# Kernel tuning notes

Hardware: AMD Instinct MI355X
Metric: run time of the kernel (lower is better)

Reference implementation:

```python
import jax, jax.numpy as jnp
import numpy as np

B, T = 4, 2048
N_EMBD = 1024
TIME_EMBD = 128
N_HEAD = 16
C_IN = N_EMBD + TIME_EMBD  # 1152


def setup_inputs() -> dict:
    key = jax.random.key(0)
    ks = jax.random.split(key, 7)
    s_in = 1.0 / np.sqrt(C_IN)
    s_e = 1.0 / np.sqrt(N_EMBD)
    return {
        "x": jax.random.normal(ks[0], (B, T, C_IN), jnp.float32),
        "ln_w": jnp.ones((C_IN,), jnp.float32),
        "ln_b": jnp.zeros((C_IN,), jnp.float32),
        "W_attn": jax.random.normal(ks[1], (C_IN, 3 * N_EMBD), jnp.float32) * s_in,
        "b_attn": jax.random.normal(ks[2], (3 * N_EMBD,), jnp.float32) * 0.01,
        "W_proj": jax.random.normal(ks[3], (N_EMBD, N_EMBD), jnp.float32) * s_e,
        "b_proj": jax.random.normal(ks[4], (N_EMBD,), jnp.float32) * 0.01,
    }


def _layernorm(x, w, b, eps=1e-5):
    mu = jnp.mean(x, axis=-1, keepdims=True)
    var = jnp.var(x, axis=-1, keepdims=True)
    return (x - mu) * jax.lax.rsqrt(var + eps) * w + b


def reference(x, ln_w, ln_b, W_attn, b_attn, W_proj, b_proj):
    h = _layernorm(x, ln_w, ln_b)                      # [B,T,C_IN]
    qkv = h @ W_attn + b_attn                          # [B,T,3*N_EMBD]
    q, k, v = jnp.split(qkv, 3, axis=-1)
    hd = N_EMBD // N_HEAD
    q = q.reshape(B, T, N_HEAD, hd).transpose(0, 2, 1, 3)  # [B,H,T,hd]
    k = k.reshape(B, T, N_HEAD, hd).transpose(0, 2, 1, 3)
    v = v.reshape(B, T, N_HEAD, hd).transpose(0, 2, 1, 3)
    att = jnp.einsum("bhqd,bhkd->bhqk", q, k) * (1.0 / np.sqrt(hd))
    mask = jnp.tril(jnp.ones((T, T), bool))
    att = jnp.where(mask, att, -jnp.inf)
    att = jax.nn.softmax(att, axis=-1)                 # dropout p=0 -> identity
    y = jnp.einsum("bhqk,bhkd->bhqd", att, v)          # [B,H,T,hd]
    y = y.transpose(0, 2, 1, 3).reshape(B, T, N_EMBD)
    return y @ W_proj + b_proj
```

## Files before the change

kernel.cpp:

```cpp
#include <hip/hip_runtime.h>
#include <hip/hip_bf16.h>

#define BB 4
#define TT 2048
#define C_IN 1152
#define NE 1024
#define NH 16
#define HD 64
#define MM (BB*TT)
#define N_QKV (3*NE)

typedef __attribute__((ext_vector_type(8))) short s16x8;
typedef __attribute__((ext_vector_type(4))) float f32x4;

static __device__ __forceinline__ unsigned short f2bf(float x) {
    unsigned int u = __float_as_uint(x);
    unsigned int r = (u + 0x7fffu + ((u >> 16) & 1u)) >> 16;
    return (unsigned short)r;
}

static __device__ __forceinline__ void async16(const void* g, void* l) {
    __builtin_amdgcn_global_load_lds((const __attribute__((address_space(1))) void*)g,
                                     (__attribute__((address_space(3))) void*)l, 16, 0, 0);
}

__global__ __launch_bounds__(256) void ln_kernel(const float* __restrict__ x,
                                                 const float* __restrict__ w,
                                                 const float* __restrict__ b,
                                                 unsigned short* __restrict__ h) {
    const int row = blockIdx.x;
    const float* xr = x + (size_t)row * C_IN;
    float s = 0.f, sq = 0.f;
    for (int i = threadIdx.x; i < C_IN; i += 256) {
        float v = xr[i];
        s += v; sq += v * v;
    }
    for (int off = 1; off < 64; off <<= 1) {
        s  += __shfl_xor(s, off, 64);
        sq += __shfl_xor(sq, off, 64);
    }
    __shared__ float red[2][4];
    const int wid = threadIdx.x >> 6, lane = threadIdx.x & 63;
    if (lane == 0) { red[0][wid] = s; red[1][wid] = sq; }
    __syncthreads();
    s  = red[0][0] + red[0][1] + red[0][2] + red[0][3];
    sq = red[1][0] + red[1][1] + red[1][2] + red[1][3];
    const float mu  = s * (1.f / C_IN);
    const float var = sq * (1.f / C_IN) - mu * mu;
    const float rs  = rsqrtf(var + 1e-5f);
    unsigned short* hr = h + (size_t)row * C_IN;
    for (int i = threadIdx.x; i < C_IN; i += 256) {
        float v = (xr[i] - mu) * rs * w[i] + b[i];
        hr[i] = f2bf(v);
    }
}

__global__ __launch_bounds__(256) void transpose_cast(const float* __restrict__ in,
                                                      unsigned short* __restrict__ out,
                                                      int K, int N) {
    __shared__ float tile[32][33];
    const int n0 = blockIdx.x * 32, k0 = blockIdx.y * 32;
    const int tx = threadIdx.x & 31, ty = threadIdx.x >> 5;
    for (int i = ty; i < 32; i += 8)
        tile[i][tx] = in[(size_t)(k0 + i) * N + n0 + tx];
    __syncthreads();
    for (int i = ty; i < 32; i += 8)
        out[(size_t)(n0 + i) * K + k0 + tx] = f2bf(tile[tx][i]);
}

#define ATT_SC 0.18033688011112042f

#define EP_STRIDE 136
template <int MODE>
__global__ __launch_bounds__(256) void gemm_bt(const unsigned short* __restrict__ A,
                                               const unsigned short* __restrict__ Bt,
                                               const float* __restrict__ bias,
                                               void* __restrict__ outp,
                                               unsigned short* __restrict__ kb,
                                               unsigned short* __restrict__ vt,
                                               int M, int N, int K) {
    __shared__ unsigned short smem[16384];
    unsigned short* As = smem;
    unsigned short* Bs = smem + 8192;
    const int tid = threadIdx.x;
    const int wid = tid >> 6, lane = tid & 63;
    const int wm = wid >> 1, wn = wid & 1;
    const int quad = lane >> 4, l16 = lane & 15;

    const int gx  = gridDim.x;
    const int nwg = gx * gridDim.y;
    const int bid = blockIdx.y * gx + blockIdx.x;
    const int wg  = (bid & 7) * (nwg >> 3) + (bid >> 3);
    const int m0 = (wg / gx) * 128, n0 = (wg % gx) * 128;

    const int srow = wid * 32 + (lane >> 2);
    const int scol = (lane & 3) * 8;
    const unsigned short* gA = A  + (size_t)(m0 + srow) * K + scol;
    const unsigned short* gB = Bt + (size_t)(n0 + srow) * K + scol;
    const int lofs = (wid * 32) * 32;

    f32x4 acc[4][4] = {};

    async16(gA,          &As[lofs]);
    async16(gA + 16 * K, &As[lofs + 16 * 32]);
    async16(gB,          &Bs[lofs]);
    async16(gB + 16 * K, &Bs[lofs + 16 * 32]);

    const int nk = K >> 5;
    for (int kt = 0; kt < nk; kt++) {
        __syncthreads();
        const int cur = kt & 1;
        if (kt + 1 < nk) {
            const int kk = (kt + 1) << 5;
            const int nxt = (cur ^ 1) * 4096;
            async16(gA + kk,          &As[nxt + lofs]);
            async16(gA + kk + 16 * K, &As[nxt + lofs + 16 * 32]);
            async16(gB + kk,          &Bs[nxt + lofs]);
            async16(gB + kk + 16 * K, &Bs[nxt + lofs + 16 * 32]);
        }
        const int cb = cur * 4096;
        s16x8 af[4], bfb[4];
        for (int mi = 0; mi < 4; mi++)
            af[mi] = *(const s16x8*)&As[cb + (wm * 64 + mi * 16 + l16) * 32 + quad * 8];
        for (int ni = 0; ni < 4; ni++)
            bfb[ni] = *(const s16x8*)&Bs[cb + (wn * 64 + ni * 16 + l16) * 32 + quad * 8];
        for (int mi = 0; mi < 4; mi++)
            for (int ni = 0; ni < 4; ni++)
                acc[mi][ni] = __builtin_amdgcn_mfma_f32_16x16x32_bf16(af[mi], bfb[ni], acc[mi][ni], 0, 0, 0);
    }

    const int which0 = n0 >> 10;
    const float sc = (MODE == 0 && which0 == 0) ? ATT_SC : 1.0f;
    for (int ni = 0; ni < 4; ni++) {
        const float bv = bias[n0 + wn * 64 + ni * 16 + l16];
        for (int mi = 0; mi < 4; mi++)
            for (int r = 0; r < 4; r++)
                acc[mi][ni][r] = (acc[mi][ni][r] + bv) * sc;
    }

    if (MODE == 1) {
        for (int mi = 0; mi < 4; mi++) {
            const int mbase = m0 + wm * 64 + mi * 16 + quad * 4;
            for (int ni = 0; ni < 4; ni++) {
                const int n_g = n0 + wn * 64 + ni * 16 + l16;
                for (int r = 0; r < 4; r++)
                    ((float*)outp)[(size_t)(mbase + r) * N + n_g] = acc[mi][ni][r];
            }
        }
        return;
    }

    const int which = n0 >> 10;
    const int bb = m0 >> 11;
    const int mloc = m0 & 2047;
    unsigned short* T = smem;

    if (which < 2) {
        unsigned short* qk = (which == 0) ? (unsigned short*)outp : kb;
        for (int pass = 0; pass < 2; pass++) {
            __syncthreads();
            if (wm == pass) {
                for (int mi = 0; mi < 4; mi++)
                    for (int ni = 0; ni < 4; ni++) {
                        const int nl = wn * 64 + ni * 16 + l16;
                        for (int r = 0; r < 4; r++)
                            T[(mi * 16 + quad * 4 + r) * EP_STRIDE + nl] = f2bf(acc[mi][ni][r]);
                    }
            }
            __syncthreads();
            const int ml = tid >> 2, c = tid & 3;
            const int t  = mloc + pass * 64 + ml;
            const int nl0 = c * 32;
            const int hh = ((n0 & 1023) >> 6) + (nl0 >> 6);
            const int d0 = nl0 & 63;
            unsigned short* dst = qk + ((size_t)(bb * 16 + hh) * TT + t) * HD + d0;
            const unsigned short* src = &T[ml * EP_STRIDE + nl0];
            for (int u = 0; u < 4; u++)
                *(s16x8*)(dst + u * 8) = *(const s16x8*)(src + u * 8);
        }
    } else {
        for (int pass = 0; pass < 2; pass++) {
            __syncthreads();
            if (wn == pass) {
                for (int mi = 0; mi < 4; mi++)
                    for (int ni = 0; ni < 4; ni++) {
                        const int nlh = ni * 16 + l16;
                        const int mlb = wm * 64 + mi * 16 + quad * 4;
                        for (int r = 0; r < 4; r += 2) {
                            const unsigned int pk = (unsigned int)f2bf(acc[mi][ni][r]) |
                                                    ((unsigned int)f2bf(acc[mi][ni][r + 1]) << 16);
                            *(unsigned int*)&T[nlh * EP_STRIDE + mlb + r] = pk;
                        }
                    }
            }
            __syncthreads();
            const int nlh = tid >> 2, c = tid & 3;
            const int hh = (n0 - 2048 + pass * 64) >> 6;
            unsigned short* dst = vt + ((size_t)(bb * 16 + hh) * HD + nlh) * TT + mloc + c * 32;
            const unsigned short* src = &T[nlh * EP_STRIDE + c * 32];
            for (int u = 0; u < 4; u++)
                *(s16x8*)(dst + u * 8) = *(const s16x8*)(src + u * 8);
        }
    }
}

#define PST 72

__global__ __launch_bounds__(256) void attn_kernel(const unsigned short* __restrict__ qb,
                                                   const unsigned short* __restrict__ kb,
                                                   const unsigned short* __restrict__ vt,
                                                   unsigned short* __restrict__ yb) {
    __shared__ unsigned short Ks[3][64 * 64];
    __shared__ unsigned short Vs[3][64 * 64];
    __shared__ unsigned short Ps[4][2 * 16 * PST];
    const int tid = threadIdx.x, wid = tid >> 6, lane = tid & 63;
    const int quad = lane >> 4, l16 = lane & 15;
    const int bh = blockIdx.x & 63;
    const int qblk = 15 - (blockIdx.x >> 6);

    const unsigned short* qh = qb + (size_t)bh * TT * HD;
    const unsigned short* kh = kb + (size_t)bh * TT * HD;
    const unsigned short* vh = vt + (size_t)bh * HD * TT;
    unsigned short* ps = Ps[wid];

    const int q0w = qblk * 128 + wid * 32;
    s16x8 aq[2][2];
    #pragma unroll
    for (int mf = 0; mf < 2; mf++) {
        aq[mf][0] = *(const s16x8*)&qh[(size_t)(q0w + mf * 16 + l16) * HD + quad * 8];
        aq[mf][1] = *(const s16x8*)&qh[(size_t)(q0w + mf * 16 + l16) * HD + 32 + quad * 8];
    }
    s16x8 onesf;
    #pragma unroll
    for (int i = 0; i < 8; i++) onesf[i] = (short)0x3F80;

    f32x4 yacc[2][4] = {};
    f32x4 lacc[2] = {};
    const int ntiles = 2 * qblk + 2;

    const int rl = lane >> 3;
    const int cc = (lane & 7) ^ (rl & 7);
    const unsigned short* kp0 = kh + (size_t)(wid * 16 + rl) * HD + cc * 8;
    const unsigned short* kp1 = kh + (size_t)(wid * 16 + 8 + rl) * HD + cc * 8;
    const unsigned short* vp0 = vh + (size_t)(wid * 16 + rl) * TT + cc * 8;
    const unsigned short* vp1 = vh + (size_t)(wid * 16 + 8 + rl) * TT + cc * 8;
    const int ldsK0 = wid * 16 * 64, ldsK1 = (wid * 16 + 8) * 64;

    async16(kp0, &Ks[0][ldsK0]);  async16(kp1, &Ks[0][ldsK1]);
    async16(vp0, &Vs[0][ldsK0]);  async16(vp1, &Vs[0][ldsK1]);
    kp0 += 64 * HD; kp1 += 64 * HD; vp0 += 64; vp1 += 64;
    async16(kp0, &Ks[1][ldsK0]);  async16(kp1, &Ks[1][ldsK1]);
    async16(vp0, &Vs[1][ldsK0]);  async16(vp1, &Vs[1][ldsK1]);
    kp0 += 64 * HD; kp1 += 64 * HD; vp0 += 64; vp1 += 64;

    const int p0s = quad ^ (l16 & 7);
    const int p1s = (4 + quad) ^ (l16 & 7);

    int bsel = 0;
    for (int t = 0; t < ntiles; ++t) {
        if (t + 1 < ntiles) { asm volatile("s_waitcnt vmcnt(4)" ::: "memory"); }
        else                { asm volatile("s_waitcnt vmcnt(0)" ::: "memory"); }
        __builtin_amdgcn_s_barrier();
        if (t + 2 < ntiles) {
            const int wsel = (bsel == 0) ? 2 : bsel - 1;
            async16(kp0, &Ks[wsel][ldsK0]);  async16(kp1, &Ks[wsel][ldsK1]);
            async16(vp0, &Vs[wsel][ldsK0]);  async16(vp1, &Vs[wsel][ldsK1]);
            kp0 += 64 * HD; kp1 += 64 * HD; vp0 += 64; vp1 += 64;
        }
        const int tk0 = t * 64;
        if (tk0 <= q0w + 31) {
            const unsigned short* Kc = Ks[bsel];
            const unsigned short* Vc = Vs[bsel];
            s16x8 kf[4][2], vf[4][2];
            #pragma unroll
            for (int nj = 0; nj < 4; nj++) {
                kf[nj][0] = *(const s16x8*)&Kc[(nj * 16 + l16) * 64 + p0s * 8];
                kf[nj][1] = *(const s16x8*)&Kc[(nj * 16 + l16) * 64 + p1s * 8];
            }
            #pragma unroll
            for (int ni = 0; ni < 4; ni++) {
                vf[ni][0] = *(const s16x8*)&Vc[(ni * 16 + l16) * 64 + p0s * 8];
                vf[ni][1] = *(const s16x8*)&Vc[(ni * 16 + l16) * 64 + p1s * 8];
            }
            #pragma unroll
            for (int mf = 0; mf < 2; mf++) {
                const int f0 = q0w + mf * 16;
                unsigned short* pm = ps + mf * (16 * PST);
                const int qg = f0 + l16;
                f32x4 st[4];
                #pragma unroll
                for (int nj = 0; nj < 4; nj++) {
                    f32x4 z = {};
                    z = __builtin_amdgcn_mfma_f32_16x16x32_bf16(kf[nj][0], aq[mf][0], z, 0, 0, 0);
                    z = __builtin_amdgcn_mfma_f32_16x16x32_bf16(kf[nj][1], aq[mf][1], z, 0, 0, 0);
                    st[nj] = z;
                }
                const bool diag = (tk0 + 64 > f0);
                #pragma unroll
                for (int nj = 0; nj < 4; nj++) {
                    const int keyb = tk0 + nj * 16 + quad * 4;
                    float pv[4];
                    #pragma unroll
                    for (int r = 0; r < 4; r++) {
                        float p = exp2f(st[nj][r]);
                        if (diag && (keyb + r > qg)) p = 0.f;
                        pv[r] = p;
                    }
                    const unsigned int pk0 = __builtin_amdgcn_perm(
                        __float_as_uint(pv[1]), __float_as_uint(pv[0]), 0x07060302u);
                    const unsigned int pk1 = __builtin_amdgcn_perm(
                        __float_as_uint(pv[3]), __float_as_uint(pv[2]), 0x07060302u);
                    *(uint2*)&pm[l16 * PST + nj * 16 + quad * 4] = make_uint2(pk0, pk1);
                }
            }
            __asm volatile("s_waitcnt lgkmcnt(0)" ::: "memory");
            __builtin_amdgcn_s_setprio(1);
            #pragma unroll
            for (int mf = 0; mf < 2; mf++) {
                unsigned short* pm = ps + mf * (16 * PST);
                const s16x8 ap0 = *(const s16x8*)&pm[l16 * PST + quad * 8];
                const s16x8 ap1 = *(const s16x8*)&pm[l16 * PST + 32 + quad * 8];
                lacc[mf] = __builtin_amdgcn_mfma_f32_16x16x32_bf16(ap0, onesf, lacc[mf], 0, 0, 0);
                lacc[mf] = __builtin_amdgcn_mfma_f32_16x16x32_bf16(ap1, onesf, lacc[mf], 0, 0, 0);
                #pragma unroll
                for (int ni = 0; ni < 4; ni++) {
                    yacc[mf][ni] = __builtin_amdgcn_mfma_f32_16x16x32_bf16(ap0, vf[ni][0], yacc[mf][ni], 0, 0, 0);
                    yacc[mf][ni] = __builtin_amdgcn_mfma_f32_16x16x32_bf16(ap1, vf[ni][1], yacc[mf][ni], 0, 0, 0);
                }
            }
            __builtin_amdgcn_s_setprio(0);
        }
        bsel = (bsel == 2) ? 0 : bsel + 1;
    }

    const int bbi = bh >> 4, hh = bh & 15;
    #pragma unroll
    for (int mf = 0; mf < 2; mf++) {
        float linv[4];
        #pragma unroll
        for (int r = 0; r < 4; r++)
            linv[r] = 1.0f / lacc[mf][r];
        #pragma unroll
        for (int ni = 0; ni < 4; ni++)
            #pragma unroll
            for (int r = 0; r < 4; r++) {
                const int trow = q0w + mf * 16 + quad * 4 + r;
                yb[((size_t)bbi * TT + trow) * NE + hh * HD + ni * 16 + l16] =
                    f2bf(yacc[mf][ni][r] * linv[r]);
            }
    }
}

extern "C" void kernel_launch(void* const* d_in, const int* in_sizes, int n_in,
                              void* d_out, int out_size, void* d_ws, size_t ws_size,
                              hipStream_t stream) {
    const float* x      = (const float*)d_in[0];
    const float* ln_w   = (const float*)d_in[1];
    const float* ln_b   = (const float*)d_in[2];
    const float* W_attn = (const float*)d_in[3];
    const float* b_attn = (const float*)d_in[4];
    const float* W_proj = (const float*)d_in[5];
    const float* b_proj = (const float*)d_in[6];
    float* out = (float*)d_out;

    char* ws = (char*)d_ws;
    unsigned short* h    = (unsigned short*)ws;  ws += (size_t)MM * C_IN * 2;
    unsigned short* Wat  = (unsigned short*)ws;  ws += (size_t)N_QKV * C_IN * 2;
    unsigned short* Wpt  = (unsigned short*)ws;  ws += (size_t)NE * NE * 2;
    unsigned short* qbuf = (unsigned short*)ws;  ws += (size_t)MM * NE * 2;
    unsigned short* kbuf = (unsigned short*)ws;  ws += (size_t)MM * NE * 2;
    unsigned short* vtbf = (unsigned short*)ws;  ws += (size_t)MM * NE * 2;
    unsigned short* ybuf = (unsigned short*)ws;  ws += (size_t)MM * NE * 2;

    ln_kernel<<<MM, 256, 0, stream>>>(x, ln_w, ln_b, h);
    transpose_cast<<<dim3(N_QKV / 32, C_IN / 32), 256, 0, stream>>>(W_attn, Wat, C_IN, N_QKV);
    transpose_cast<<<dim3(NE / 32, NE / 32), 256, 0, stream>>>(W_proj, Wpt, NE, NE);
    gemm_bt<0><<<dim3(N_QKV / 128, MM / 128), 256, 0, stream>>>(h, Wat, b_attn, qbuf, kbuf, vtbf,
                                                                MM, N_QKV, C_IN);
    attn_kernel<<<64 * 16, 256, 0, stream>>>(qbuf, kbuf, vtbf, ybuf);
    gemm_bt<1><<<dim3(NE / 128, MM / 128), 256, 0, stream>>>(ybuf, Wpt, b_proj, out, nullptr, nullptr,
                                                             MM, NE, NE);
}
```

Measured before the change: 310.6 us.

## Restructure attention into single-wave blocks loading K/V directly into registers

The attention kernel changes from 4-wave blocks with a triple-buffered async LDS pipeline for K/V to single-wave blocks of 32 queries each, launched on a 4096-block grid. K and V fragments are read straight from global memory into registers, and the next K tile is prefetched after the QK MFMAs. Barriers, shared K/V staging and the per-tile causal skip checks go away, and the masked and unmasked exp paths are split. In exchange, K/V reuse through LDS across the four waves is lost, so global and L2 traffic per query roughly quadruples, and V loads are exposed without a software pipeline.

```diff
diff --git a/kernel.cpp b/kernel.cpp
--- a/kernel.cpp
+++ b/kernel.cpp
@@ -206,24 +206,21 @@
 
 #define PST 72
 
-__global__ __launch_bounds__(256) void attn_kernel(const unsigned short* __restrict__ qb,
-                                                   const unsigned short* __restrict__ kb,
-                                                   const unsigned short* __restrict__ vt,
-                                                   unsigned short* __restrict__ yb) {
-    __shared__ unsigned short Ks[3][64 * 64];
-    __shared__ unsigned short Vs[3][64 * 64];
-    __shared__ unsigned short Ps[4][2 * 16 * PST];
-    const int tid = threadIdx.x, wid = tid >> 6, lane = tid & 63;
+__global__ __launch_bounds__(64, 3) void attn_kernel(const unsigned short* __restrict__ qb,
+                                                     const unsigned short* __restrict__ kb,
+                                                     const unsigned short* __restrict__ vt,
+                                                     unsigned short* __restrict__ yb) {
+    __shared__ unsigned short Ps[2 * 16 * PST];
+    const int lane = threadIdx.x;
     const int quad = lane >> 4, l16 = lane & 15;
-    const int bh = blockIdx.x & 63;
-    const int qblk = 15 - (blockIdx.x >> 6);
+    const int bid = blockIdx.x;
+    const int bh = bid & 63;
+    const int q0w = (63 - (bid >> 6)) * 32;
 
     const unsigned short* qh = qb + (size_t)bh * TT * HD;
     const unsigned short* kh = kb + (size_t)bh * TT * HD;
     const unsigned short* vh = vt + (size_t)bh * HD * TT;
-    unsigned short* ps = Ps[wid];
-
-    const int q0w = qblk * 128 + wid * 32;
+
     s16x8 aq[2][2];
     #pragma unroll
     for (int mf = 0; mf < 2; mf++) {
@@ -236,101 +233,89 @@
 
     f32x4 yacc[2][4] = {};
     f32x4 lacc[2] = {};
-    const int ntiles = 2 * qblk + 2;
-
-    const int rl = lane >> 3;
-    const int cc = (lane & 7) ^ (rl & 7);
-    const unsigned short* kp0 = kh + (size_t)(wid * 16 + rl) * HD + cc * 8;
-    const unsigned short* kp1 = kh + (size_t)(wid * 16 + 8 + rl) * HD + cc * 8;
-    const unsigned short* vp0 = vh + (size_t)(wid * 16 + rl) * TT + cc * 8;
-    const unsigned short* vp1 = vh + (size_t)(wid * 16 + 8 + rl) * TT + cc * 8;
-    const int ldsK0 = wid * 16 * 64, ldsK1 = (wid * 16 + 8) * 64;
-
-    async16(kp0, &Ks[0][ldsK0]);  async16(kp1, &Ks[0][ldsK1]);
-    async16(vp0, &Vs[0][ldsK0]);  async16(vp1, &Vs[0][ldsK1]);
-    kp0 += 64 * HD; kp1 += 64 * HD; vp0 += 64; vp1 += 64;
-    async16(kp0, &Ks[1][ldsK0]);  async16(kp1, &Ks[1][ldsK1]);
-    async16(vp0, &Vs[1][ldsK0]);  async16(vp1, &Vs[1][ldsK1]);
-    kp0 += 64 * HD; kp1 += 64 * HD; vp0 += 64; vp1 += 64;
-
-    const int p0s = quad ^ (l16 & 7);
-    const int p1s = (4 + quad) ^ (l16 & 7);
-
-    int bsel = 0;
-    for (int t = 0; t < ntiles; ++t) {
-        if (t + 1 < ntiles) { asm volatile("s_waitcnt vmcnt(4)" ::: "memory"); }
-        else                { asm volatile("s_waitcnt vmcnt(0)" ::: "memory"); }
-        __builtin_amdgcn_s_barrier();
-        if (t + 2 < ntiles) {
-            const int wsel = (bsel == 0) ? 2 : bsel - 1;
-            async16(kp0, &Ks[wsel][ldsK0]);  async16(kp1, &Ks[wsel][ldsK1]);
-            async16(vp0, &Vs[wsel][ldsK0]);  async16(vp1, &Vs[wsel][ldsK1]);
-            kp0 += 64 * HD; kp1 += 64 * HD; vp0 += 64; vp1 += 64;
-        }
+    const int nact = (q0w >> 6) + 1;
+
+    const unsigned short* kfp = kh + (size_t)l16 * HD + quad * 8;
+    const unsigned short* vfp = vh + (size_t)l16 * TT + quad * 8;
+
+    s16x8 kf[4][2], vf[4][2];
+    #pragma unroll
+    for (int nj = 0; nj < 4; nj++) {
+        kf[nj][0] = *(const s16x8*)(kfp + (size_t)(nj * 16) * HD);
+        kf[nj][1] = *(const s16x8*)(kfp + (size_t)(nj * 16) * HD + 32);
+    }
+
+    for (int t = 0; t < nact; ++t) {
         const int tk0 = t * 64;
-        if (tk0 <= q0w + 31) {
-            const unsigned short* Kc = Ks[bsel];
-            const unsigned short* Vc = Vs[bsel];
-            s16x8 kf[4][2], vf[4][2];
+
+        #pragma unroll
+        for (int ni = 0; ni < 4; ni++) {
+            const unsigned short* vp = vfp + (size_t)(ni * 16) * TT + tk0;
+            vf[ni][0] = *(const s16x8*)(vp);
+            vf[ni][1] = *(const s16x8*)(vp + 32);
+        }
+
+        f32x4 st[2][4];
+        #pragma unroll
+        for (int mf = 0; mf < 2; mf++)
             #pragma unroll
             for (int nj = 0; nj < 4; nj++) {
-                kf[nj][0] = *(const s16x8*)&Kc[(nj * 16 + l16) * 64 + p0s * 8];
-                kf[nj][1] = *(const s16x8*)&Kc[(nj * 16 + l16) * 64 + p1s * 8];
-            }
+                f32x4 z = {};
+                z = __builtin_amdgcn_mfma_f32_16x16x32_bf16(kf[nj][0], aq[mf][0], z, 0, 0, 0);
+                z = __builtin_amdgcn_mfma_f32_16x16x32_bf16(kf[nj][1], aq[mf][1], z, 0, 0, 0);
+                st[mf][nj] = z;
+            }
+
+        if (t + 1 < nact) {
+            const unsigned short* kp = kfp + (size_t)(tk0 + 64) * HD;
+            #pragma unroll
+            for (int nj = 0; nj < 4; nj++) {
+                kf[nj][0] = *(const s16x8*)(kp + (size_t)(nj * 16) * HD);
+                kf[nj][1] = *(const s16x8*)(kp + (size_t)(nj * 16) * HD + 32);
+            }
+        }
+
+#define EXP_STORE(MASKED)                                                              \
+        _Pragma("unroll")                                                              \
+        for (int mf = 0; mf < 2; mf++) {                                               \
+            unsigned short* pm = Ps + mf * (16 * PST);                                 \
+            const int qg = q0w + mf * 16 + l16;                                        \
+            _Pragma("unroll")                                                          \
+            for (int nj = 0; nj < 4; nj++) {                                           \
+                const int keyb = tk0 + nj * 16 + quad * 4;                             \
+                float pv[4];                                                           \
+                _Pragma("unroll")                                                      \
+                for (int r = 0; r < 4; r++) {                                          \
+                    float p = exp2f(st[mf][nj][r]);                                    \
+                    if (MASKED && (keyb + r > qg)) p = 0.f;                            \
+                    pv[r] = p;                                                         \
+                }                                                                      \
+                const unsigned int pk0 = __builtin_amdgcn_perm(                        \
+                    __float_as_uint(pv[1]), __float_as_uint(pv[0]), 0x07060302u);      \
+                const unsigned int pk1 = __builtin_amdgcn_perm(                        \
+                    __float_as_uint(pv[3]), __float_as_uint(pv[2]), 0x07060302u);      \
+                *(uint2*)&pm[l16 * PST + nj * 16 + quad * 4] = make_uint2(pk0, pk1);   \
+            }                                                                          \
+        }
+        if (tk0 + 64 > q0w) { EXP_STORE(1) } else { EXP_STORE(0) }
+#undef EXP_STORE
+
+        __asm volatile("s_waitcnt lgkmcnt(0)" ::: "memory");
+        __builtin_amdgcn_s_setprio(1);
+        #pragma unroll
+        for (int mf = 0; mf < 2; mf++) {
+            unsigned short* pm = Ps + mf * (16 * PST);
+            const s16x8 ap0 = *(const s16x8*)&pm[l16 * PST + quad * 8];
+            const s16x8 ap1 = *(const s16x8*)&pm[l16 * PST + 32 + quad * 8];
+            lacc[mf] = __builtin_amdgcn_mfma_f32_16x16x32_bf16(ap0, onesf, lacc[mf], 0, 0, 0);
+            lacc[mf] = __builtin_amdgcn_mfma_f32_16x16x32_bf16(ap1, onesf, lacc[mf], 0, 0, 0);
             #pragma unroll
             for (int ni = 0; ni < 4; ni++) {
-                vf[ni][0] = *(const s16x8*)&Vc[(ni * 16 + l16) * 64 + p0s * 8];
-                vf[ni][1] = *(const s16x8*)&Vc[(ni * 16 + l16) * 64 + p1s * 8];
-            }
-            #pragma unroll
-            for (int mf = 0; mf < 2; mf++) {
-                const int f0 = q0w + mf * 16;
-                unsigned short* pm = ps + mf * (16 * PST);
-                const int qg = f0 + l16;
-                f32x4 st[4];
-                #pragma unroll
-                for (int nj = 0; nj < 4; nj++) {
-                    f32x4 z = {};
-                    z = __builtin_amdgcn_mfma_f32_16x16x32_bf16(kf[nj][0], aq[mf][0], z, 0, 0, 0);
-                    z = __builtin_amdgcn_mfma_f32_16x16x32_bf16(kf[nj][1], aq[mf][1], z, 0, 0, 0);
-                    st[nj] = z;
-                }
-                const bool diag = (tk0 + 64 > f0);
-                #pragma unroll
-                for (int nj = 0; nj < 4; nj++) {
-                    const int keyb = tk0 + nj * 16 + quad * 4;
-                    float pv[4];
-                    #pragma unroll
-                    for (int r = 0; r < 4; r++) {
-                        float p = exp2f(st[nj][r]);
-                        if (diag && (keyb + r > qg)) p = 0.f;
-                        pv[r] = p;
-                    }
-                    const unsigned int pk0 = __builtin_amdgcn_perm(
-                        __float_as_uint(pv[1]), __float_as_uint(pv[0]), 0x07060302u);
-                    const unsigned int pk1 = __builtin_amdgcn_perm(
-                        __float_as_uint(pv[3]), __float_as_uint(pv[2]), 0x07060302u);
-                    *(uint2*)&pm[l16 * PST + nj * 16 + quad * 4] = make_uint2(pk0, pk1);
-                }
-            }
-            __asm volatile("s_waitcnt lgkmcnt(0)" ::: "memory");
-            __builtin_amdgcn_s_setprio(1);
-            #pragma unroll
-            for (int mf = 0; mf < 2; mf++) {
-                unsigned short* pm = ps + mf * (16 * PST);
-                const s16x8 ap0 = *(const s16x8*)&pm[l16 * PST + quad * 8];
-                const s16x8 ap1 = *(const s16x8*)&pm[l16 * PST + 32 + quad * 8];
-                lacc[mf] = __builtin_amdgcn_mfma_f32_16x16x32_bf16(ap0, onesf, lacc[mf], 0, 0, 0);
-                lacc[mf] = __builtin_amdgcn_mfma_f32_16x16x32_bf16(ap1, onesf, lacc[mf], 0, 0, 0);
-                #pragma unroll
-                for (int ni = 0; ni < 4; ni++) {
-                    yacc[mf][ni] = __builtin_amdgcn_mfma_f32_16x16x32_bf16(ap0, vf[ni][0], yacc[mf][ni], 0, 0, 0);
-                    yacc[mf][ni] = __builtin_amdgcn_mfma_f32_16x16x32_bf16(ap1, vf[ni][1], yacc[mf][ni], 0, 0, 0);
-                }
-            }
-            __builtin_amdgcn_s_setprio(0);
-        }
-        bsel = (bsel == 2) ? 0 : bsel + 1;
+                yacc[mf][ni] = __builtin_amdgcn_mfma_f32_16x16x32_bf16(ap0, vf[ni][0], yacc[mf][ni], 0, 0, 0);
+                yacc[mf][ni] = __builtin_amdgcn_mfma_f32_16x16x32_bf16(ap1, vf[ni][1], yacc[mf][ni], 0, 0, 0);
+            }
+        }
+        __builtin_amdgcn_s_setprio(0);
     }
 
     const int bbi = bh >> 4, hh = bh & 15;
@@ -377,7 +362,7 @@
     transpose_cast<<<dim3(NE / 32, NE / 32), 256, 0, stream>>>(W_proj, Wpt, NE, NE);
     gemm_bt<0><<<dim3(N_QKV / 128, MM / 128), 256, 0, stream>>>(h, Wat, b_attn, qbuf, kbuf, vtbf,
                                                                 MM, N_QKV, C_IN);
-    attn_kernel<<<64 * 16, 256, 0, stream>>>(qbuf, kbuf, vtbf, ybuf);
+    attn_kernel<<<64 * 64, 64, 0, stream>>>(qbuf, kbuf, vtbf, ybuf);
     gemm_bt<1><<<dim3(NE / 128, MM / 128), 256, 0, stream>>>(ybuf, Wpt, b_proj, out, nullptr, nullptr,
                                                              MM, NE, NE);
 }
```

After: 350.3 us. 1.13x slower.
